# Kernel optimization log

Hardware: AMD Instinct MI355X
Metric: run time of the kernel (lower is better)

## Reference

```python
import jax, jax.numpy as jnp
import numpy as np

B, V, L = 2, 12000, 16
IN_F = 479  # 3+3+3+9+3+10+64+256(imgf)+128(gar_latent)


def setup_inputs() -> dict:
    key = jax.random.key(0)
    ks = jax.random.split(key, 12)

    def w(k, shape, fan_in):
        return (jax.random.normal(k, shape, jnp.float32) / np.sqrt(fan_in)).astype(jnp.float32)

    return {
        "x": jax.random.normal(ks[0], (B, V, IN_F), jnp.float32),
        "spiral_idx": jax.random.randint(ks[1], (V + 1, L), 0, V + 1),  # indices incl. dummy vertex V
        "W_point": w(ks[2], (IN_F, 256), IN_F),                 # pointMLP Linear, no bias
        "res1_W": w(ks[3], (2, 256 * L, 256), 256 * L),          # two SpiralConv(256,256)
        "res1_b": jnp.zeros((2, 256), jnp.float32),
        "W_mid": w(ks[4], (256, 128), 256),                      # midDown, no bias
        "ress_W": w(ks[5], (3, 2, 128 * L, 128), 128 * L),       # 3 residual blocks of SpiralConv(128,128)
        "ress_b": jnp.zeros((3, 2, 128), jnp.float32),
        "Wo1": w(ks[6], (512, 256), 512), "bo1": jnp.zeros((256,), jnp.float32),
        "Wo2": w(ks[7], (256, 128), 256), "bo2": jnp.zeros((128,), jnp.float32),
        "Wo3": w(ks[8], (128, 3), 128),  "bo3": jnp.zeros((3,), jnp.float32),
    }


def _spiral_conv(x, idx, Wc, bc, zp):
    # x: [B, Vp, C]; idx: [Vp, L] -> gather spiral neighborhoods then linear, mask dummy vertex
    Bn, Vp, C = x.shape
    g = x[:, idx.reshape(-1), :].reshape(Bn, Vp, -1)  # [B, Vp, L*C]
    return (g @ Wc + bc) * zp


def _res_block(x, idx, Wb, bb, zp):
    h = jax.nn.relu(_spiral_conv(x, idx, Wb[0], bb[0], zp))
    h = _spiral_conv(h, idx, Wb[1], bb[1], zp)
    return jax.nn.relu(h + x)


def reference(x, spiral_idx, W_point, res1_W, res1_b, W_mid, ress_W, ress_b,
              Wo1, bo1, Wo2, bo2, Wo3, bo3):
    pf = jax.nn.relu(x @ W_point)                                  # [B, V, 256]
    Bn = pf.shape[0]
    pfs = jnp.concatenate([pf, jnp.zeros((Bn, 1, pf.shape[-1]), pf.dtype)], axis=1)  # [B, V+1, 256]
    Vp = pfs.shape[1]
    zp = jnp.ones((1, Vp, 1), pf.dtype).at[0, -1, 0].set(0.0)       # zero_padding mask
    fs = (_res_block(pfs, spiral_idx, res1_W, res1_b, zp) @ W_mid) * zp  # [B, Vp, 128]
    gfs = jnp.max(fs[:, :-1, :], axis=1, keepdims=True)             # masked global max-pool [B,1,128]
    for i in range(3):
        fs = _res_block(fs, spiral_idx, ress_W[i], ress_b[i], zp)
    g = jnp.broadcast_to(gfs, (Bn, Vp, gfs.shape[-1])) * zp
    h = jnp.concatenate([pfs, fs, g], axis=-1)                      # [B, Vp, 512]
    h = jax.nn.relu(h @ Wo1 + bo1)
    h = jax.nn.relu(h @ Wo2 + bo2)
    out = h @ Wo3 + bo3
    return out[:, :-1, :]                                           # drop dummy vertex
```

## Files before the change

kernel.cpp:

```cpp
#include <hip/hip_runtime.h>
#include <cstdint>
#include <cfloat>
#include <cstddef>

constexpr int BATCH  = 2;
constexpr int V      = 12000;
constexpr int VP     = V + 1;
constexpr int M_ROWS = BATCH * VP;
constexpr int L_SP   = 16;

typedef _Float16 half_t;
typedef _Float16 half8 __attribute__((ext_vector_type(8)));
typedef float floatx4 __attribute__((ext_vector_type(4)));

__device__ __forceinline__ void async_cp16(const void* g, void* l) {
    __builtin_amdgcn_global_load_lds(
        (const __attribute__((address_space(1))) unsigned int*)g,
        (__attribute__((address_space(3))) unsigned int*)l, 16, 0, 0);
}

template<bool GATHER, int BM, int BN, int LGC>
__global__ __launch_bounds__(256, 4)
void gemm_mfma(const half_t* __restrict__ A, const half_t* __restrict__ Wt,
               const float* __restrict__ bias, const half_t* __restrict__ res,
               const int* __restrict__ idx, half_t* __restrict__ out,
               int M, int N, int K, int KA, int relu, int mask)
{
    constexpr int AI = (BM >= 32) ? (BM / 32) : 1;
    constexpr int NB = BN / 32;
    constexpr int WROWS = (BM >= 32) ? 2 : 1;
    constexpr int AFR = (BM / WROWS) / 16;
    constexpr int BFR = (BN / (4 / WROWS)) / 16;
    __shared__ half_t As[BM * 64];
    __shared__ half_t Bs[BN * 64];

    const int tid  = threadIdx.x;
    const int lane = tid & 63;
    const int w    = tid >> 6;
    const int bm   = blockIdx.x, bn = blockIdx.y;

    const int goff = (((lane & 7) ^ ((lane >> 3) & 7)) << 3);
    const int rsub = lane >> 3;

    const half_t* wp[NB];
    half_t* lB[NB];
#pragma unroll
    for (int bi = 0; bi < NB; ++bi) {
        const int blk = w + (bi << 2);
        wp[bi] = Wt + (size_t)(bn * BN + (blk << 3) + rsub) * K + goff;
        lB[bi] = &Bs[(size_t)((blk << 6) + lane) * 8];
    }

    const bool astage = (BM >= 32) || (tid < 128);
    int vv[AI], abase[AI];
    const half_t* aP[AI];
    half_t* lA[AI];
#pragma unroll
    for (int ai = 0; ai < AI; ++ai) {
        const int blk = w + (ai << 2);
        int m = bm * BM + (blk << 3) + rsub;
        if (m >= M) m = M - 1;
        const int b = m / VP;
        vv[ai] = m - b * VP;
        abase[ai] = b * VP;
        aP[ai] = GATHER ? nullptr : (A + (size_t)m * KA + goff);
        lA[ai] = &As[(size_t)(((blk << 6) + lane) & (BM * 8 - 1)) * 8];
    }

    const int wm = (WROWS == 2) ? (w >> 1) * (BM / 2) : 0;
    const int wn = (WROWS == 2) ? (w & 1) * (BN / 2) : w * (BN / 4);
    const int fr = lane & 15;
    const int q  = lane >> 4;
    const int f7 = fr & 7;

    floatx4 acc[AFR][BFR] = {};

    auto compute = [&]() {
#pragma unroll
        for (int s = 0; s < 2; ++s) {
            const int ck = ((((s << 2) | q) ^ f7) << 3);
            half8 af[AFR], bf[BFR];
#pragma unroll
            for (int i = 0; i < AFR; ++i)
                af[i] = *(const half8*)&As[(wm + (i << 4) + fr) * 64 + ck];
#pragma unroll
            for (int j = 0; j < BFR; ++j)
                bf[j] = *(const half8*)&Bs[(wn + (j << 4) + fr) * 64 + ck];
#pragma unroll
            for (int i = 0; i < AFR; ++i)
#pragma unroll
                for (int j = 0; j < BFR; ++j)
                    acc[i][j] = __builtin_amdgcn_mfma_f32_16x16x32_f16(af[i], bf[j], acc[i][j], 0, 0, 0);
        }
    };

    if (GATHER) {
        constexpr int NI = (1 << LGC) >> 6;
        constexpr int L  = 16;
        int jc[AI], jn[AI];
#pragma unroll
        for (int ai = 0; ai < AI; ++ai) jc[ai] = idx[vv[ai] << 4];
#pragma unroll
        for (int ai = 0; ai < AI; ++ai) jn[ai] = idx[(vv[ai] << 4) + 1];
#pragma unroll 1
        for (int l = 0; l < L; ++l) {
            const half_t* g[AI];
#pragma unroll
            for (int ai = 0; ai < AI; ++ai)
                g[ai] = A + (((size_t)(abase[ai] + jc[ai])) << LGC) + goff;
            const int kb = l << LGC;
#pragma unroll
            for (int kc = 0; kc < NI; ++kc) {
                if (astage) {
#pragma unroll
                    for (int ai = 0; ai < AI; ++ai)
                        async_cp16(g[ai] + (kc << 6), lA[ai]);
                }
#pragma unroll
                for (int bi = 0; bi < NB; ++bi)
                    async_cp16(wp[bi] + kb + (kc << 6), lB[bi]);
                __syncthreads();
                compute();
                __syncthreads();
            }
#pragma unroll
            for (int ai = 0; ai < AI; ++ai) jc[ai] = jn[ai];
            if (l + 2 < L) {
#pragma unroll
                for (int ai = 0; ai < AI; ++ai) jn[ai] = idx[(vv[ai] << 4) + l + 2];
            }
        }
    } else {
        const int nk = K >> 6;
        for (int t = 0; t < nk; ++t) {
            const int k0 = t << 6;
            if (astage) {
#pragma unroll
                for (int ai = 0; ai < AI; ++ai)
                    async_cp16(aP[ai] + k0, lA[ai]);
            }
#pragma unroll
            for (int bi = 0; bi < NB; ++bi)
                async_cp16(wp[bi] + k0, lB[bi]);
            __syncthreads();
            compute();
            __syncthreads();
        }
    }

    const int er = q << 2;
#pragma unroll
    for (int i = 0; i < AFR; ++i) {
#pragma unroll
        for (int j = 0; j < BFR; ++j) {
            const int n = bn * BN + wn + (j << 4) + fr;
            const floatx4 a = acc[i][j];
#pragma unroll
            for (int r = 0; r < 4; ++r) {
                const int m = bm * BM + wm + (i << 4) + er + r;
                if (m >= M) continue;
                float val = a[r];
                if (bias) val += bias[n];
                if (res)  val += (float)res[(size_t)m * N + n];
                if (relu) val = fmaxf(val, 0.f);
                const int vvm = m - (m / VP) * VP;
                if (mask && vvm == VP - 1) val = 0.f;
                out[(size_t)m * N + n] = (half_t)val;
            }
        }
    }
}

__global__ void wcvt(const float* __restrict__ in, half_t* __restrict__ out,
                     int K, int N, int Kpad)
{
    __shared__ float t[32][33];
    const size_t ioff = (size_t)blockIdx.z * K * N;
    const size_t ooff = (size_t)blockIdx.z * N * Kpad;
    const int k0 = blockIdx.x * 32, n0 = blockIdx.y * 32;
    const int tx = threadIdx.x & 31, ty = threadIdx.x >> 5;
#pragma unroll
    for (int r = 0; r < 4; ++r) {
        const int k = k0 + ty + r * 8;
        t[ty + r * 8][tx] = (k < K && n0 + tx < N) ? in[ioff + (size_t)k * N + n0 + tx] : 0.f;
    }
    __syncthreads();
#pragma unroll
    for (int r = 0; r < 4; ++r) {
        const int n = n0 + ty + r * 8;
        const int k = k0 + tx;
        if (n < N && k < Kpad) out[ooff + (size_t)n * Kpad + k] = (half_t)t[tx][ty + r * 8];
    }
}

__global__ void cvt_x(const float* __restrict__ x, half_t* __restrict__ xh)
{
    const int m = blockIdx.x;
    const int b = m / VP, v = m - b * VP;
    for (int k = threadIdx.x; k < 512; k += 256) {
        float val = (v < V && k < 479) ? x[((size_t)b * V + v) * 479 + k] : 0.f;
        xh[(size_t)m * 512 + k] = (half_t)val;
    }
}

__global__ void maxpool1(const half_t* __restrict__ fs, float* __restrict__ pmax)
{
    const int b = blockIdx.x, chunk = blockIdx.y;
    const int c = threadIdx.x;
    const int v0 = chunk * (V / 32);
    float m = -FLT_MAX;
    const half_t* p = fs + ((size_t)b * VP + v0) * 128 + c;
    for (int v = 0; v < V / 32; ++v) { m = fmaxf(m, (float)*p); p += 128; }
    pmax[((size_t)b * 32 + chunk) * 128 + c] = m;
}
__global__ void maxpool2(const float* __restrict__ pmax, half_t* __restrict__ gfs)
{
    const int b = blockIdx.x, c = threadIdx.x;
    float m = -FLT_MAX;
    for (int i = 0; i < 32; ++i) m = fmaxf(m, pmax[((size_t)b * 32 + i) * 128 + c]);
    gfs[b * 128 + c] = (half_t)m;
}

__global__ void concat_k(const half_t* __restrict__ pfs, const half_t* __restrict__ fs,
                         const half_t* __restrict__ gfs, half_t* __restrict__ h)
{
    const size_t i = (size_t)blockIdx.x * 256 + threadIdx.x;
    if (i >= (size_t)M_ROWS * 512) return;
    const int    n   = (int)(i & 511);
    const size_t row = i >> 9;
    const int    b   = (int)(row / VP);
    const int    v   = (int)(row - (size_t)b * VP);
    half_t val;
    if (n < 256)      val = pfs[row * 256 + n];
    else if (n < 384) val = fs[row * 128 + (n - 256)];
    else              val = (v == VP - 1) ? (half_t)0.f : gfs[b * 128 + (n - 384)];
    h[i] = val;
}

__global__ void final_k(const half_t* __restrict__ h, const float* __restrict__ Wo3,
                        const float* __restrict__ bo3, float* __restrict__ out)
{
    __shared__ float wsm[384];
    __shared__ float b3[3];
    for (int t = threadIdx.x; t < 384; t += 256) wsm[t] = Wo3[t];
    if (threadIdx.x < 3) b3[threadIdx.x] = bo3[threadIdx.x];
    __syncthreads();

    const int gid = blockIdx.x * 256 + threadIdx.x;
    if (gid >= BATCH * V) return;
    const int b = gid / V;
    const int v = gid - b * V;
    const half_t* hr = h + ((size_t)b * VP + v) * 128;

    float o0 = b3[0], o1 = b3[1], o2 = b3[2];
#pragma unroll 4
    for (int c = 0; c < 128; ++c) {
        const float hv = (float)hr[c];
        o0 += hv * wsm[c * 3 + 0];
        o1 += hv * wsm[c * 3 + 1];
        o2 += hv * wsm[c * 3 + 2];
    }
    out[(size_t)gid * 3 + 0] = o0;
    out[(size_t)gid * 3 + 1] = o1;
    out[(size_t)gid * 3 + 2] = o2;
}

extern "C" void kernel_launch(void* const* d_in, const int* in_sizes, int n_in,
                              void* d_out, int out_size, void* d_ws, size_t ws_size,
                              hipStream_t stream)
{
    const float* x       = (const float*)d_in[0];
    const int*   sidx    = (const int*)  d_in[1];
    const float* W_point = (const float*)d_in[2];
    const float* res1_W  = (const float*)d_in[3];
    const float* res1_b  = (const float*)d_in[4];
    const float* W_mid   = (const float*)d_in[5];
    const float* ress_W  = (const float*)d_in[6];
    const float* ress_b  = (const float*)d_in[7];
    const float* Wo1     = (const float*)d_in[8];
    const float* bo1     = (const float*)d_in[9];
    const float* Wo2     = (const float*)d_in[10];
    const float* bo2     = (const float*)d_in[11];
    const float* Wo3     = (const float*)d_in[12];
    const float* bo3     = (const float*)d_in[13];
    float* out = (float*)d_out;

    char* p = (char*)d_ws;
    auto alloc = [&](size_t bytes) { char* q = p; p += (bytes + 255) & ~(size_t)255; return q; };
    const size_t fs_bytes = (size_t)M_ROWS * 128 * 2;
    half_t* reg0 = (half_t*)alloc((size_t)M_ROWS * 512 * 2);
    half_t* pfs  = (half_t*)alloc((size_t)M_ROWS * 256 * 2);
    char*   rA   = alloc((size_t)M_ROWS * 256 * 2);
    char*   rB   = alloc((size_t)M_ROWS * 256 * 2);
    half_t* Wpt_t  = (half_t*)alloc((size_t)256 * 512 * 2);
    half_t* r1Wt   = (half_t*)alloc((size_t)2 * 256 * 4096 * 2);
    half_t* Wmid_t = (half_t*)alloc((size_t)128 * 256 * 2);
    half_t* rsWt   = (half_t*)alloc((size_t)6 * 128 * 2048 * 2);
    half_t* Wo1_t  = (half_t*)alloc((size_t)256 * 512 * 2);
    half_t* Wo2_t  = (half_t*)alloc((size_t)128 * 256 * 2);
    float*  pmax   = (float*)alloc((size_t)2 * 32 * 128 * 4);
    half_t* gfs    = (half_t*)alloc(512);

    half_t* bufA = (half_t*)rA;
    half_t* bufB = (half_t*)rB;
    half_t* fsA  = (half_t*)rA;
    half_t* fsB  = (half_t*)(rA + fs_bytes);
    half_t* tmp  = (half_t*)rB;
    half_t* h512 = reg0;
    half_t* h256 = (half_t*)rB;
    half_t* h128 = (half_t*)rA;

    const dim3 blk(256);

    wcvt<<<dim3(16, 8, 1),  blk, 0, stream>>>(W_point, Wpt_t, 479, 256, 512);
    wcvt<<<dim3(128, 8, 2), blk, 0, stream>>>(res1_W, r1Wt, 4096, 256, 4096);
    wcvt<<<dim3(8, 4, 1),   blk, 0, stream>>>(W_mid, Wmid_t, 256, 128, 256);
    wcvt<<<dim3(64, 4, 6),  blk, 0, stream>>>(ress_W, rsWt, 2048, 128, 2048);
    wcvt<<<dim3(16, 8, 1),  blk, 0, stream>>>(Wo1, Wo1_t, 512, 256, 512);
    wcvt<<<dim3(8, 4, 1),   blk, 0, stream>>>(Wo2, Wo2_t, 256, 128, 256);
    cvt_x<<<M_ROWS, blk, 0, stream>>>(x, reg0);

    const int mg64 = (M_ROWS + 63) / 64;
    const int mg32 = (M_ROWS + 31) / 32;
    const int mg16 = (M_ROWS + 15) / 16;

    gemm_mfma<false, 64, 64, 0><<<dim3(mg64, 4), blk, 0, stream>>>(
        reg0, Wpt_t, nullptr, nullptr, nullptr, pfs,
        M_ROWS, 256, 512, 512, 1, 1);

    gemm_mfma<true, 64, 64, 8><<<dim3(mg64, 4), blk, 0, stream>>>(
        pfs, r1Wt, res1_b, nullptr, sidx, bufA,
        M_ROWS, 256, 4096, 0, 1, 1);

    gemm_mfma<true, 64, 64, 8><<<dim3(mg64, 4), blk, 0, stream>>>(
        bufA, r1Wt + (size_t)256 * 4096, res1_b + 256, pfs, sidx, bufB,
        M_ROWS, 256, 4096, 0, 1, 1);

    gemm_mfma<false, 32, 64, 0><<<dim3(mg32, 2), blk, 0, stream>>>(
        bufB, Wmid_t, nullptr, nullptr, nullptr, fsA,
        M_ROWS, 128, 256, 256, 0, 1);

    maxpool1<<<dim3(BATCH, 32), dim3(128), 0, stream>>>(fsA, pmax);
    maxpool2<<<dim3(BATCH), dim3(128), 0, stream>>>(pmax, gfs);

    half_t* cur = fsA;
    half_t* nxt = fsB;
    for (int i = 0; i < 3; ++i) {
        const half_t* Wa = rsWt + (size_t)(2 * i + 0) * 128 * 2048;
        const half_t* Wb = rsWt + (size_t)(2 * i + 1) * 128 * 2048;
        const float* ba = ress_b + (2 * i + 0) * 128;
        const float* bb = ress_b + (2 * i + 1) * 128;
        gemm_mfma<true, 16, 128, 7><<<dim3(mg16, 1), blk, 0, stream>>>(
            cur, Wa, ba, nullptr, sidx, tmp,
            M_ROWS, 128, 2048, 0, 1, 1);
        gemm_mfma<true, 16, 128, 7><<<dim3(mg16, 1), blk, 0, stream>>>(
            tmp, Wb, bb, cur, sidx, nxt,
            M_ROWS, 128, 2048, 0, 1, 1);
        half_t* t2 = cur; cur = nxt; nxt = t2;
    }

    concat_k<<<(unsigned)(((size_t)M_ROWS * 512 + 255) / 256), blk, 0, stream>>>(
        pfs, cur, gfs, h512);

    gemm_mfma<false, 64, 64, 0><<<dim3(mg64, 4), blk, 0, stream>>>(
        h512, Wo1_t, bo1, nullptr, nullptr, h256,
        M_ROWS, 256, 512, 512, 1, 0);

    gemm_mfma<false, 32, 64, 0><<<dim3(mg32, 2), blk, 0, stream>>>(
        h256, Wo2_t, bo2, nullptr, nullptr, h128,
        M_ROWS, 128, 256, 256, 1, 0);

    final_k<<<(BATCH * V + 255) / 256, blk, 0, stream>>>(h128, Wo3, bo3, out);
}
```

Before: 693.7 us.

## Swizzle gather GEMM blocks across XCDs by batch and retile residual convs

The spiral-conv gather GEMMs now remap block IDs so that each group of XCDs handles a single batch's vertex tiles. Gathered neighbour rows of one batch then stay within a shared L2, and tiles no longer straddle the batch boundary. The 128-channel residual convs change from 16x128 tiles with half the threads staging A to 32x64 tiles over two N-blocks, and the BM<32 special-casing is removed. The trade-offs are some wasted rows in each batch's last tile and twice the gather traffic for the 128-channel layers, since the A tile is reloaded per N-block.

```diff
diff --git a/kernel.cpp b/kernel.cpp
--- a/kernel.cpp
+++ b/kernel.cpp
@@ -19,25 +19,33 @@
         (__attribute__((address_space(3))) unsigned int*)l, 16, 0, 0);
 }
 
-template<bool GATHER, int BM, int BN, int LGC>
+template<bool GATHER, int BM, int BN, int LGC, bool XSWZ>
 __global__ __launch_bounds__(256, 4)
 void gemm_mfma(const half_t* __restrict__ A, const half_t* __restrict__ Wt,
                const float* __restrict__ bias, const half_t* __restrict__ res,
                const int* __restrict__ idx, half_t* __restrict__ out,
                int M, int N, int K, int KA, int relu, int mask)
 {
-    constexpr int AI = (BM >= 32) ? (BM / 32) : 1;
+    constexpr int AI = BM / 32;
     constexpr int NB = BN / 32;
-    constexpr int WROWS = (BM >= 32) ? 2 : 1;
-    constexpr int AFR = (BM / WROWS) / 16;
-    constexpr int BFR = (BN / (4 / WROWS)) / 16;
+    constexpr int AFR = (BM / 2) / 16;
+    constexpr int BFR = (BN / 2) / 16;
     __shared__ half_t As[BM * 64];
     __shared__ half_t Bs[BN * 64];
 
     const int tid  = threadIdx.x;
     const int lane = tid & 63;
     const int w    = tid >> 6;
-    const int bm   = blockIdx.x, bn = blockIdx.y;
+    const int bn   = blockIdx.y;
+
+    int tile, batch;
+    if (XSWZ) {
+        const int xcd = blockIdx.x & 7, slot = blockIdx.x >> 3;
+        batch = xcd >> 2;
+        tile  = slot * 4 + (xcd & 3);
+    } else {
+        tile = blockIdx.x; batch = 0;
+    }
 
     const int goff = (((lane & 7) ^ ((lane >> 3) & 7)) << 3);
     const int rsub = lane >> 3;
@@ -51,24 +59,28 @@
         lB[bi] = &Bs[(size_t)((blk << 6) + lane) * 8];
     }
 
-    const bool astage = (BM >= 32) || (tid < 128);
     int vv[AI], abase[AI];
     const half_t* aP[AI];
     half_t* lA[AI];
 #pragma unroll
     for (int ai = 0; ai < AI; ++ai) {
         const int blk = w + (ai << 2);
-        int m = bm * BM + (blk << 3) + rsub;
-        if (m >= M) m = M - 1;
-        const int b = m / VP;
-        vv[ai] = m - b * VP;
-        abase[ai] = b * VP;
-        aP[ai] = GATHER ? nullptr : (A + (size_t)m * KA + goff);
-        lA[ai] = &As[(size_t)(((blk << 6) + lane) & (BM * 8 - 1)) * 8];
-    }
-
-    const int wm = (WROWS == 2) ? (w >> 1) * (BM / 2) : 0;
-    const int wn = (WROWS == 2) ? (w & 1) * (BN / 2) : w * (BN / 4);
+        const int r = (blk << 3) + rsub;
+        if (XSWZ) {
+            int v = tile * BM + r; if (v >= VP) v = VP - 1;
+            vv[ai] = v; abase[ai] = batch * VP;
+            aP[ai] = nullptr;
+        } else {
+            int m = tile * BM + r; if (m >= M) m = M - 1;
+            const int b = m / VP;
+            vv[ai] = m - b * VP; abase[ai] = b * VP;
+            aP[ai] = GATHER ? nullptr : (A + (size_t)m * KA + goff);
+        }
+        lA[ai] = &As[(size_t)((blk << 6) + lane) * 8];
+    }
+
+    const int wm = (w >> 1) * (BM / 2);
+    const int wn = (w & 1) * (BN / 2);
     const int fr = lane & 15;
     const int q  = lane >> 4;
     const int f7 = fr & 7;
@@ -111,11 +123,9 @@
             const int kb = l << LGC;
 #pragma unroll
             for (int kc = 0; kc < NI; ++kc) {
-                if (astage) {
-#pragma unroll
-                    for (int ai = 0; ai < AI; ++ai)
-                        async_cp16(g[ai] + (kc << 6), lA[ai]);
-                }
+#pragma unroll
+                for (int ai = 0; ai < AI; ++ai)
+                    async_cp16(g[ai] + (kc << 6), lA[ai]);
 #pragma unroll
                 for (int bi = 0; bi < NB; ++bi)
                     async_cp16(wp[bi] + kb + (kc << 6), lB[bi]);
@@ -134,11 +144,9 @@
         const int nk = K >> 6;
         for (int t = 0; t < nk; ++t) {
             const int k0 = t << 6;
-            if (astage) {
-#pragma unroll
-                for (int ai = 0; ai < AI; ++ai)
-                    async_cp16(aP[ai] + k0, lA[ai]);
-            }
+#pragma unroll
+            for (int ai = 0; ai < AI; ++ai)
+                async_cp16(aP[ai] + k0, lA[ai]);
 #pragma unroll
             for (int bi = 0; bi < NB; ++bi)
                 async_cp16(wp[bi] + k0, lB[bi]);
@@ -157,13 +165,19 @@
             const floatx4 a = acc[i][j];
 #pragma unroll
             for (int r = 0; r < 4; ++r) {
-                const int m = bm * BM + wm + (i << 4) + er + r;
-                if (m >= M) continue;
+                int m, vvm;
+                const int mr = tile * BM + wm + (i << 4) + er + r;
+                if (XSWZ) {
+                    vvm = mr < VP ? mr : VP - 1;
+                    m = batch * VP + vvm;
+                } else {
+                    if (mr >= M) continue;
+                    m = mr; vvm = m - (m / VP) * VP;
+                }
                 float val = a[r];
                 if (bias) val += bias[n];
                 if (res)  val += (float)res[(size_t)m * N + n];
                 if (relu) val = fmaxf(val, 0.f);
-                const int vvm = m - (m / VP) * VP;
                 if (mask && vvm == VP - 1) val = 0.f;
                 out[(size_t)m * N + n] = (half_t)val;
             }
@@ -322,21 +336,22 @@
 
     const int mg64 = (M_ROWS + 63) / 64;
     const int mg32 = (M_ROWS + 31) / 32;
-    const int mg16 = (M_ROWS + 15) / 16;
-
-    gemm_mfma<false, 64, 64, 0><<<dim3(mg64, 4), blk, 0, stream>>>(
+    const int sg64 = 2 * ((VP + 63) / 64);
+    const int sg32 = 2 * ((VP + 31) / 32);
+
+    gemm_mfma<false, 64, 64, 0, false><<<dim3(mg64, 4), blk, 0, stream>>>(
         reg0, Wpt_t, nullptr, nullptr, nullptr, pfs,
         M_ROWS, 256, 512, 512, 1, 1);
 
-    gemm_mfma<true, 64, 64, 8><<<dim3(mg64, 4), blk, 0, stream>>>(
+    gemm_mfma<true, 64, 64, 8, true><<<dim3(sg64, 4), blk, 0, stream>>>(
         pfs, r1Wt, res1_b, nullptr, sidx, bufA,
         M_ROWS, 256, 4096, 0, 1, 1);
 
-    gemm_mfma<true, 64, 64, 8><<<dim3(mg64, 4), blk, 0, stream>>>(
+    gemm_mfma<true, 64, 64, 8, true><<<dim3(sg64, 4), blk, 0, stream>>>(
         bufA, r1Wt + (size_t)256 * 4096, res1_b + 256, pfs, sidx, bufB,
         M_ROWS, 256, 4096, 0, 1, 1);
 
-    gemm_mfma<false, 32, 64, 0><<<dim3(mg32, 2), blk, 0, stream>>>(
+    gemm_mfma<false, 32, 64, 0, false><<<dim3(mg32, 2), blk, 0, stream>>>(
         bufB, Wmid_t, nullptr, nullptr, nullptr, fsA,
         M_ROWS, 128, 256, 256, 0, 1);
 
@@ -350,10 +365,10 @@
         const half_t* Wb = rsWt + (size_t)(2 * i + 1) * 128 * 2048;
         const float* ba = ress_b + (2 * i + 0) * 128;
         const float* bb = ress_b + (2 * i + 1) * 128;
-        gemm_mfma<true, 16, 128, 7><<<dim3(mg16, 1), blk, 0, stream>>>(
+        gemm_mfma<true, 32, 64, 7, true><<<dim3(sg32, 2), blk, 0, stream>>>(
             cur, Wa, ba, nullptr, sidx, tmp,
             M_ROWS, 128, 2048, 0, 1, 1);
-        gemm_mfma<true, 16, 128, 7><<<dim3(mg16, 1), blk, 0, stream>>>(
+        gemm_mfma<true, 32, 64, 7, true><<<dim3(sg32, 2), blk, 0, stream>>>(
             tmp, Wb, bb, cur, sidx, nxt,
             M_ROWS, 128, 2048, 0, 1, 1);
         half_t* t2 = cur; cur = nxt; nxt = t2;
@@ -362,11 +377,11 @@
     concat_k<<<(unsigned)(((size_t)M_ROWS * 512 + 255) / 256), blk, 0, stream>>>(
         pfs, cur, gfs, h512);
 
-    gemm_mfma<false, 64, 64, 0><<<dim3(mg64, 4), blk, 0, stream>>>(
+    gemm_mfma<false, 64, 64, 0, false><<<dim3(mg64, 4), blk, 0, stream>>>(
         h512, Wo1_t, bo1, nullptr, nullptr, h256,
         M_ROWS, 256, 512, 512, 1, 0);
 
-    gemm_mfma<false, 32, 64, 0><<<dim3(mg32, 2), blk, 0, stream>>>(
+    gemm_mfma<false, 32, 64, 0, false><<<dim3(mg32, 2), blk, 0, stream>>>(
         h256, Wo2_t, bo2, nullptr, nullptr, h128,
         M_ROWS, 128, 256, 256, 1, 0);
 
```

Result: faster. 574.4 us (-17.2%).
